# Performance work log

Hardware: AMD Instinct MI355X
Metric: run time of the kernel (lower is better)

## Reference

```python
import jax, jax.numpy as jnp
import numpy as np

NPOINT, RADIUS, NSAMPLE = 1024, 0.2, 32
BN_EPS = 1e-5


def _fps(xyz, npoint):
    """Farthest point sampling. xyz: [B,N,3] -> idx [B,npoint]. Deterministic seed (point 0)."""
    B, N, _ = xyz.shape
    init = (jnp.full((B, N), 1e10, xyz.dtype), jnp.zeros((B,), jnp.int32))

    def step(carry, _):
        distance, farthest = carry
        centroid = jnp.take_along_axis(xyz, farthest[:, None, None], axis=1)  # [B,1,3]
        dist = jnp.sum((xyz - centroid) ** 2, -1)                              # [B,N]
        distance = jnp.minimum(distance, dist)
        nxt = jnp.argmax(distance, axis=-1).astype(jnp.int32)
        return (distance, nxt), farthest

    _, cents = jax.lax.scan(step, init, None, length=npoint)  # [npoint,B]
    return cents.T  # [B,npoint]


def _gather(points, idx):
    """points [B,N,C], idx [B,...] -> [B,...,C] (batched fancy indexing)."""
    return jax.vmap(lambda p, i: p[i])(points, idx)


def _square_distance(src, dst):
    # [B,S,3] x [B,N,3] -> [B,S,N]
    d = -2.0 * jnp.einsum('bsc,bnc->bsn', src, dst)
    d += jnp.sum(src ** 2, -1)[:, :, None]
    d += jnp.sum(dst ** 2, -1)[:, None, :]
    return d


def _query_ball(radius, nsample, xyz, new_xyz):
    B, N, _ = xyz.shape
    sqr = _square_distance(new_xyz, xyz)                      # [B,S,N]
    base = jnp.arange(N, dtype=jnp.int32)[None, None, :]
    idx = jnp.where(sqr > radius ** 2, N, base)
    idx = jnp.sort(idx, axis=-1)[:, :, :nsample]              # [B,S,K]
    first = idx[:, :, 0:1]
    idx = jnp.where(idx == N, first, idx)
    return jnp.clip(idx, 0, N - 1)


def _mlp_bn_relu(h, w, b, g, be):
    # h: [B,S,K,Cin]; 1x1 conv == matmul; BN (training-mode batch stats) over (B,S,K).
    y = jnp.einsum('bskc,cd->bskd', h, w) + b
    mu = jnp.mean(y, axis=(0, 1, 2))
    var = jnp.var(y, axis=(0, 1, 2))
    y = (y - mu) * jax.lax.rsqrt(var + BN_EPS) * g + be
    return jax.nn.relu(y)


def setup_inputs():
    key = jax.random.key(0)
    ks = jax.random.split(key, 8)
    B, N, D = 16, 4096, 64
    xyz = jax.random.uniform(ks[0], (B, 3, N), jnp.float32)           # points in unit cube
    points = jax.random.normal(ks[1], (B, D, N), jnp.float32)
    c = [3 + D, 64, 64, 128]
    w0 = jax.random.normal(ks[2], (c[0], c[1]), jnp.float32) * 0.1
    w1 = jax.random.normal(ks[3], (c[1], c[2]), jnp.float32) * 0.1
    w2 = jax.random.normal(ks[4], (c[2], c[3]), jnp.float32) * 0.1
    b0 = jax.random.normal(ks[5], (c[1],), jnp.float32) * 0.05
    b1 = jax.random.normal(ks[6], (c[2],), jnp.float32) * 0.05
    b2 = jax.random.normal(ks[7], (c[3],), jnp.float32) * 0.05
    return dict(xyz=xyz, points=points,
                w0=w0, b0=b0, g0=jnp.ones(c[1]), be0=jnp.zeros(c[1]),
                w1=w1, b1=b1, g1=jnp.ones(c[2]), be1=jnp.zeros(c[2]),
                w2=w2, b2=b2, g2=jnp.ones(c[3]), be2=jnp.zeros(c[3]))


def reference(xyz, points, w0, b0, g0, be0, w1, b1, g1, be1, w2, b2, g2, be2):
    xyz_t = jnp.transpose(xyz, (0, 2, 1))       # [B,N,3]
    pts_t = jnp.transpose(points, (0, 2, 1))    # [B,N,D]
    B, N, _ = xyz_t.shape

    fps_idx = _fps(xyz_t, NPOINT)                               # [B,S]
    new_xyz = _gather(xyz_t, fps_idx)                           # [B,S,3]
    idx = _query_ball(RADIUS, NSAMPLE, xyz_t, new_xyz)          # [B,S,K]
    grouped_xyz = _gather(xyz_t, idx) - new_xyz[:, :, None, :]  # [B,S,K,3]
    grouped_pts = _gather(pts_t, idx)                           # [B,S,K,D]
    h = jnp.concatenate([grouped_xyz, grouped_pts], axis=-1)    # [B,S,K,3+D]

    h = _mlp_bn_relu(h, w0, b0, g0, be0)
    h = _mlp_bn_relu(h, w1, b1, g1, be1)
    h = _mlp_bn_relu(h, w2, b2, g2, be2)
    new_points = jnp.max(h, axis=2)                             # [B,S,Cout]

    return jnp.transpose(new_xyz, (0, 2, 1)), jnp.transpose(new_points, (0, 2, 1))
```

## Files before the change

### kernel.cpp

```cpp
#include <hip/hip_runtime.h>
#include <hip/hip_bf16.h>

typedef unsigned short u16;
typedef short short8 __attribute__((ext_vector_type(8)));
typedef float f32x4 __attribute__((ext_vector_type(4)));

#define NBLK_PASS 4096

#define WS_XYZT   0u
#define WS_PTSH   786432u
#define WS_PTSL   (WS_PTSH + 8388608u)
#define WS_NEWXYZ (WS_PTSL + 8388608u)
#define WS_BALL   (WS_NEWXYZ + 196608u)
#define WS_W0F    (WS_BALL + 2097152u)
#define WS_W1F    (WS_W0F + 24576u)
#define WS_W2F    (WS_W1F + 16384u)
#define WS_P0     (WS_W2F + 32768u)
#define WS_P1     (WS_P0 + 2097152u)
#define WS_P2     (WS_P1 + 2097152u)
#define WS_PR     (WS_P2 + 4194304u)
#define WS_AC0    (WS_PR + 65536u)
#define WS_AC1    (WS_AC0 + 1024u)
#define WS_AC2    (WS_AC1 + 1024u)

__device__ __forceinline__ void split2(float v, u16& h, u16& l) {
  __hip_bfloat16 bh = __float2bfloat16(v);
  float r = v - __bfloat162float(bh);
  __hip_bfloat16 bl = __float2bfloat16(r);
  h = *reinterpret_cast<u16*>(&bh);
  l = *reinterpret_cast<u16*>(&bl);
}

#define DPP_MAX64(CTRL) { \
  unsigned int lo_ = (unsigned int)k, hi_ = (unsigned int)(k >> 32); \
  unsigned int mlo_ = (unsigned int)__builtin_amdgcn_update_dpp(0, (int)lo_, CTRL, 0xF, 0xF, true); \
  unsigned int mhi_ = (unsigned int)__builtin_amdgcn_update_dpp(0, (int)hi_, CTRL, 0xF, 0xF, true); \
  unsigned long long m_ = ((unsigned long long)mhi_ << 32) | mlo_; \
  if (m_ > k) k = m_; }

__global__ __launch_bounds__(512) void front_k(
    const float* __restrict__ xyz, const float* __restrict__ pts,
    const float* __restrict__ w0, const float* __restrict__ w1, const float* __restrict__ w2,
    float* __restrict__ xyzT, u16* __restrict__ ptsH, u16* __restrict__ ptsL,
    float* __restrict__ newxyz, float* __restrict__ out0,
    u16* __restrict__ w0f, u16* __restrict__ w1f, u16* __restrict__ w2f)
{
  __shared__ __align__(16) char sm[53376];
  int bid = blockIdx.x, tid = threadIdx.x;

  if (bid < 16) {
    float* lx = (float*)sm; float* ly = lx + 4096; float* lz = ly + 4096;
    int* sIdx = (int*)(sm + 49152);
    unsigned long long* red = (unsigned long long*)(sm + 53248);
    int b = bid, lane = tid & 63, wid = tid >> 6;
    const float4* sx = (const float4*)(xyz + (size_t)(b*3 + 0)*4096);
    const float4* sy = (const float4*)(xyz + (size_t)(b*3 + 1)*4096);
    const float4* sz = (const float4*)(xyz + (size_t)(b*3 + 2)*4096);
    for (int i = tid; i < 1024; i += 512) {
      ((float4*)lx)[i] = sx[i]; ((float4*)ly)[i] = sy[i]; ((float4*)lz)[i] = sz[i];
    }
    __syncthreads();
    float px[8], py[8], pz[8], dist[8];
    #pragma unroll
    for (int i = 0; i < 8; ++i) {
      int p = tid + 512*i;
      px[i] = lx[p]; py[i] = ly[p]; pz[i] = lz[p]; dist[i] = 1e10f;
    }
    unsigned int lo0 = 4095u - (unsigned int)tid;
    int far = 0;
    for (int t = 0; t < 1024; ++t) {
      if (tid == 0) sIdx[t] = far;
      if (t == 1023) break;
      float cx = lx[far], cy = ly[far], cz = lz[far];
      float bestnd = -1.f; unsigned int bestlow = 0u;
      #pragma unroll
      for (int i = 0; i < 8; ++i) {
        float dx = __fsub_rn(px[i], cx);
        float dy = __fsub_rn(py[i], cy);
        float dz = __fsub_rn(pz[i], cz);
        float d = __fadd_rn(__fadd_rn(__fmul_rn(dx,dx), __fmul_rn(dy,dy)), __fmul_rn(dz,dz));
        float nd = fminf(dist[i], d);
        dist[i] = nd;
        if (nd > bestnd) { bestnd = nd; bestlow = lo0 - 512u*i; }
      }
      unsigned long long k = ((unsigned long long)__float_as_uint(bestnd) << 32) | bestlow;
      DPP_MAX64(0x111) DPP_MAX64(0x112) DPP_MAX64(0x114) DPP_MAX64(0x118)
      DPP_MAX64(0x142) DPP_MAX64(0x143)
      if (lane == 63) red[(t & 1)*8 + wid] = k;
      __syncthreads();
      const unsigned long long* rr = red + (t & 1)*8;
      unsigned long long m = rr[0];
      #pragma unroll
      for (int w = 1; w < 8; ++w) { unsigned long long o = rr[w]; if (o > m) m = o; }
      far = 4095 - (int)(unsigned int)(m & 0xffffffffull);
    }
    __syncthreads();
    for (int t = tid; t < 1024; t += 512) {
      int fi = sIdx[t];
      float x = lx[fi], y = ly[fi], z = lz[fi];
      size_t nb = ((size_t)b*1024 + t)*3;
      newxyz[nb + 0] = x; newxyz[nb + 1] = y; newxyz[nb + 2] = z;
      out0[(size_t)(b*3 + 0)*1024 + t] = x;
      out0[(size_t)(b*3 + 1)*1024 + t] = y;
      out0[(size_t)(b*3 + 2)*1024 + t] = z;
    }
  } else if (bid == 16) {
    for (int e = tid; e < 6144; e += 512) {
      int j = e & 7, l = (e >> 3) & 63, ct = (e >> 9) & 3, ks = e >> 11;
      int kk = ks*32 + (l >> 4)*8 + j, col = ct*16 + (l & 15);
      float v = 0.f;
      if (kk < 67) { int orow = (kk < 64) ? (kk + 3) : (kk - 64); v = w0[orow*64 + col]; }
      u16 h, lo; split2(v, h, lo);
      w0f[e] = h; w0f[6144 + e] = lo;
    }
    for (int e = tid; e < 4096; e += 512) {
      int j = e & 7, l = (e >> 3) & 63, ct = (e >> 9) & 3, ks = e >> 11;
      int kk = ks*32 + (l >> 4)*8 + j, col = ct*16 + (l & 15);
      u16 h, lo; split2(w1[kk*64 + col], h, lo);
      w1f[e] = h; w1f[4096 + e] = lo;
    }
    for (int e = tid; e < 8192; e += 512) {
      int j = e & 7, l = (e >> 3) & 63, ct = (e >> 9) & 3, ks = (e >> 11) & 1, cg = e >> 12;
      int kk = ks*32 + (l >> 4)*8 + j, col = cg*64 + ct*16 + (l & 15);
      u16 h, lo; split2(w2[kk*128 + col], h, lo);
      w2f[e] = h; w2f[8192 + e] = lo;
    }
  } else if (bid < 145) {
    int i = (bid - 17)*512 + tid;
    int b = i >> 12, n = i & 4095;
    float x = xyz[(b*3 + 0)*4096 + n];
    float y = xyz[(b*3 + 1)*4096 + n];
    float z = xyz[(b*3 + 2)*4096 + n];
    xyzT[(size_t)i*3 + 0] = x; xyzT[(size_t)i*3 + 1] = y; xyzT[(size_t)i*3 + 2] = z;
  } else {
    int bx = bid - 145;
    u16* th = (u16*)sm;
    u16* tl = th + 64*68;
    int b = bx >> 6, nt = bx & 63;
    int j = tid & 63, dq = tid >> 6;
    #pragma unroll
    for (int db = 0; db < 8; ++db) {
      int d = db*8 + dq;
      float v = pts[((size_t)(b*64 + d))*4096 + nt*64 + j];
      u16 h, lo; split2(v, h, lo);
      th[j*68 + d] = h; tl[j*68 + d] = lo;
    }
    __syncthreads();
    int row = tid >> 3, q = tid & 7;
    size_t o = ((size_t)(b*4096 + nt*64 + row))*64 + q*8;
    const u16* sh = th + row*68 + q*8;
    const u16* sl = tl + row*68 + q*8;
    uint2 h0 = *(const uint2*)(sh), h1 = *(const uint2*)(sh + 4);
    uint2 l0 = *(const uint2*)(sl), l1 = *(const uint2*)(sl + 4);
    *(uint2*)(ptsH + o) = h0; *(uint2*)(ptsH + o + 4) = h1;
    *(uint2*)(ptsL + o) = l0; *(uint2*)(ptsL + o + 4) = l1;
  }
}

__global__ __launch_bounds__(256) void ball_k(const float* __restrict__ xyz,
                                              const float* __restrict__ newxyz,
                                              int* __restrict__ ballidx) {
  __shared__ __align__(16) float lx[4096], ly[4096], lz[4096], ldn[4096];
  int b = blockIdx.x >> 5, tid = threadIdx.x, lane = tid & 63, wid = tid >> 6;
  const float4* sx = (const float4*)(xyz + (size_t)(b*3 + 0)*4096);
  const float4* sy = (const float4*)(xyz + (size_t)(b*3 + 1)*4096);
  const float4* sz = (const float4*)(xyz + (size_t)(b*3 + 2)*4096);
  for (int i = tid; i < 1024; i += 256) {
    ((float4*)lx)[i] = sx[i]; ((float4*)ly)[i] = sy[i]; ((float4*)lz)[i] = sz[i];
  }
  __syncthreads();
  for (int i = tid; i < 4096; i += 256) {
    float x = lx[i], y = ly[i], z = lz[i];
    ldn[i] = __fadd_rn(__fadd_rn(__fmul_rn(x,x), __fmul_rn(y,y)), __fmul_rn(z,z));
  }
  __syncthreads();
  int s0 = (blockIdx.x & 31)*32 + wid*8;
  for (int ci = 0; ci < 8; ++ci) {
    int s = s0 + ci;
    const float* cp = newxyz + ((size_t)b*1024 + s)*3;
    float cx = cp[0], cy = cp[1], cz = cp[2];
    float sn = __fadd_rn(__fadd_rn(__fmul_rn(cx,cx), __fmul_rn(cy,cy)), __fmul_rn(cz,cz));
    int* orow = ballidx + (((size_t)b << 10) + s)*32;
    int cnt = 0, first = -1;
    for (int ch = 0; ch < 64; ++ch) {
      int p = ch*64 + lane;
      float x = lx[p], y = ly[p], z = lz[p];
      float dot = __fmaf_rn(cz, z, __fmaf_rn(cy, y, __fmul_rn(cx, x)));
      float sqr = __fadd_rn(__fadd_rn(__fmul_rn(-2.0f, dot), sn), ldn[p]);
      bool in = !(sqr > 0.04f);
      unsigned long long mask = __ballot(in);
      if (first < 0 && mask) first = ch*64 + (__ffsll((long long)mask) - 1);
      int rank = cnt + __popcll(mask & ((1ull << lane) - 1ull));
      if (in && rank < 32) orow[rank] = p;
      cnt += __popcll(mask);
      if (cnt >= 32) break;
    }
    if (cnt < 32) {
      int fv = (first < 0) ? 4095 : first;
      if (lane >= cnt && lane < 32) orow[lane] = fv;
    }
  }
}

#define LOFF 6144

__device__ __forceinline__ void stats_fin(float* sSt, float* __restrict__ partial,
                                          int C, int tid, int bid) {
  __syncthreads();
  for (int c = tid; c < C; c += 256) {
    float s = sSt[c*2] + sSt[(128 + c)*2] + sSt[(256 + c)*2] + sSt[(384 + c)*2];
    float q = sSt[c*2 + 1] + sSt[(128 + c)*2 + 1] + sSt[(256 + c)*2 + 1] + sSt[(384 + c)*2 + 1];
    partial[(size_t)bid*2*C + c] = s;
    partial[(size_t)bid*2*C + C + c] = q;
  }
}

template<int DEPTH>
__global__ __launch_bounds__(256, 2) void pass_k(
    const int* __restrict__ ballidx,
    const u16* __restrict__ ptsH, const u16* __restrict__ ptsL,
    const float* __restrict__ xyzT, const float* __restrict__ newxyz,
    const u16* __restrict__ w0f, const u16* __restrict__ w1f, const u16* __restrict__ w2f,
    const float* __restrict__ b0, const float* __restrict__ b1, const float* __restrict__ b2,
    const float* __restrict__ ac0, const float* __restrict__ ac1, const float* __restrict__ ac2,
    float* __restrict__ partial, float* __restrict__ outPts)
{
  __shared__ __align__(16) u16 sAh[128*104];
  __shared__ __align__(16) u16 sAl[128*104];
  __shared__ __align__(16) u16 sW[12288];
  int tid = threadIdx.x, lane = tid & 63, wid = tid >> 6;
  int lrow = lane & 15, lkg = lane >> 4;
  int r0 = wid*32;

  {
    int r = tid >> 1, half = tid & 1;
    int R = blockIdx.x*128 + r;
    int b = R >> 15, s = (R & 32767) >> 5;
    int n = ballidx[R];
    size_t o = ((((size_t)b << 12) + n) << 6) + half*32;
    const uint4* srcH = (const uint4*)(ptsH + o);
    const uint4* srcL = (const uint4*)(ptsL + o);
    uint4* dH = (uint4*)(&sAh[r*104 + half*32]);
    uint4* dL = (uint4*)(&sAl[r*104 + half*32]);
    #pragma unroll
    for (int i = 0; i < 4; ++i) { dH[i] = srcH[i]; dL[i] = srcL[i]; }
    if (half) {
      uint4 zz; zz.x = zz.y = zz.z = zz.w = 0u;
      uint4* zH = (uint4*)(&sAh[r*104 + 64]);
      uint4* zL = (uint4*)(&sAl[r*104 + 64]);
      #pragma unroll
      for (int i = 0; i < 4; ++i) { zH[i] = zz; zL[i] = zz; }
      const float* xp = xyzT + (((size_t)b << 12) + n)*3;
      const float* cp = newxyz + (((size_t)b << 10) + s)*3;
      #pragma unroll
      for (int d = 0; d < 3; ++d) {
        u16 h, l; split2(__fsub_rn(xp[d], cp[d]), h, l);
        sAh[r*104 + 64 + d] = h; sAl[r*104 + 64 + d] = l;
      }
    }
  }
  for (int i = tid; i < 768; i += 256) {
    ((uint4*)sW)[i] = ((const uint4*)w0f)[i];
    *(uint4*)(sW + LOFF + i*8) = ((const uint4*)(w0f + 6144))[i];
  }
  __syncthreads();

  f32x4 zv = {0.f, 0.f, 0.f, 0.f};

  f32x4 acc[2][4];
  #pragma unroll
  for (int rt = 0; rt < 2; ++rt)
    #pragma unroll
    for (int ct = 0; ct < 4; ++ct) acc[rt][ct] = zv;
  #pragma unroll
  for (int ks = 0; ks < 3; ++ks) {
    short8 ah[2], al[2];
    #pragma unroll
    for (int rt = 0; rt < 2; ++rt) {
      int ro = (r0 + rt*16 + lrow)*104 + ks*32 + lkg*8;
      ah[rt] = *(const short8*)&sAh[ro];
      al[rt] = *(const short8*)&sAl[ro];
    }
    #pragma unroll
    for (int ct = 0; ct < 4; ++ct) {
      short8 wh = *(const short8*)&sW[((ks*4 + ct)*64 + lane)*8];
      short8 wl = *(const short8*)&sW[LOFF + ((ks*4 + ct)*64 + lane)*8];
      #pragma unroll
      for (int rt = 0; rt < 2; ++rt) {
        acc[rt][ct] = __builtin_amdgcn_mfma_f32_16x16x32_bf16(ah[rt], wh, acc[rt][ct], 0, 0, 0);
        acc[rt][ct] = __builtin_amdgcn_mfma_f32_16x16x32_bf16(al[rt], wh, acc[rt][ct], 0, 0, 0);
        acc[rt][ct] = __builtin_amdgcn_mfma_f32_16x16x32_bf16(ah[rt], wl, acc[rt][ct], 0, 0, 0);
      }
    }
  }

  if constexpr (DEPTH == 1) {
    __syncthreads();
    float* sSt = (float*)sW;
    #pragma unroll
    for (int ct = 0; ct < 4; ++ct) {
      int col = ct*16 + lrow;
      float bv = b0[col], s = 0.f, q = 0.f;
      #pragma unroll
      for (int rt = 0; rt < 2; ++rt)
        #pragma unroll
        for (int r = 0; r < 4; ++r) { float v = acc[rt][ct][r] + bv; s += v; q += v*v; }
      s += __shfl_xor(s, 16, 64); q += __shfl_xor(q, 16, 64);
      s += __shfl_xor(s, 32, 64); q += __shfl_xor(q, 32, 64);
      if (lane < 16) { sSt[(wid*128 + col)*2] = s; sSt[(wid*128 + col)*2 + 1] = q; }
    }
    stats_fin(sSt, partial, 64, tid, blockIdx.x);
    return;
  } else {
    __syncthreads();
    #pragma unroll
    for (int ct = 0; ct < 4; ++ct) {
      int col = ct*16 + lrow;
      float a = ac0[col], cc = fmaf(a, b0[col], ac0[64 + col]);
      #pragma unroll
      for (int rt = 0; rt < 2; ++rt)
        #pragma unroll
        for (int r = 0; r < 4; ++r) {
          float v = fmaxf(fmaf(a, acc[rt][ct][r], cc), 0.f);
          int row = r0 + rt*16 + lkg*4 + r;
          u16 h, l; split2(v, h, l);
          sAh[row*72 + col] = h; sAl[row*72 + col] = l;
        }
    }
    for (int i = tid; i < 512; i += 256) {
      ((uint4*)sW)[i] = ((const uint4*)w1f)[i];
      *(uint4*)(sW + LOFF + i*8) = ((const uint4*)(w1f + 4096))[i];
    }
    __syncthreads();

    #pragma unroll
    for (int rt = 0; rt < 2; ++rt)
      #pragma unroll
      for (int ct = 0; ct < 4; ++ct) acc[rt][ct] = zv;
    #pragma unroll
    for (int ks = 0; ks < 2; ++ks) {
      short8 ah[2], al[2];
      #pragma unroll
      for (int rt = 0; rt < 2; ++rt) {
        int ro = (r0 + rt*16 + lrow)*72 + ks*32 + lkg*8;
        ah[rt] = *(const short8*)&sAh[ro];
        al[rt] = *(const short8*)&sAl[ro];
      }
      #pragma unroll
      for (int ct = 0; ct < 4; ++ct) {
        short8 wh = *(const short8*)&sW[((ks*4 + ct)*64 + lane)*8];
        short8 wl = *(const short8*)&sW[LOFF + ((ks*4 + ct)*64 + lane)*8];
        #pragma unroll
        for (int rt = 0; rt < 2; ++rt) {
          acc[rt][ct] = __builtin_amdgcn_mfma_f32_16x16x32_bf16(ah[rt], wh, acc[rt][ct], 0, 0, 0);
          acc[rt][ct] = __builtin_amdgcn_mfma_f32_16x16x32_bf16(al[rt], wh, acc[rt][ct], 0, 0, 0);
          acc[rt][ct] = __builtin_amdgcn_mfma_f32_16x16x32_bf16(ah[rt], wl, acc[rt][ct], 0, 0, 0);
        }
      }
    }

    if constexpr (DEPTH == 2) {
      __syncthreads();
      float* sSt = (float*)sW;
      #pragma unroll
      for (int ct = 0; ct < 4; ++ct) {
        int col = ct*16 + lrow;
        float bv = b1[col], s = 0.f, q = 0.f;
        #pragma unroll
        for (int rt = 0; rt < 2; ++rt)
          #pragma unroll
          for (int r = 0; r < 4; ++r) { float v = acc[rt][ct][r] + bv; s += v; q += v*v; }
        s += __shfl_xor(s, 16, 64); q += __shfl_xor(q, 16, 64);
        s += __shfl_xor(s, 32, 64); q += __shfl_xor(q, 32, 64);
        if (lane < 16) { sSt[(wid*128 + col)*2] = s; sSt[(wid*128 + col)*2 + 1] = q; }
      }
      stats_fin(sSt, partial, 64, tid, blockIdx.x);
      return;
    } else {
      __syncthreads();
      #pragma unroll
      for (int ct = 0; ct < 4; ++ct) {
        int col = ct*16 + lrow;
        float a = ac1[col], cc = fmaf(a, b1[col], ac1[64 + col]);
        #pragma unroll
        for (int rt = 0; rt < 2; ++rt)
          #pragma unroll
          for (int r = 0; r < 4; ++r) {
            float v = fmaxf(fmaf(a, acc[rt][ct][r], cc), 0.f);
            int row = r0 + rt*16 + lkg*4 + r;
            u16 h, l; split2(v, h, l);
            sAh[row*72 + col] = h; sAl[row*72 + col] = l;
          }
      }
      for (int i = tid; i < 512; i += 256) {
        ((uint4*)sW)[i] = ((const uint4*)w2f)[i];
        *(uint4*)(sW + LOFF + i*8) = ((const uint4*)(w2f + 8192))[i];
      }
      __syncthreads();

      float sc[2][4], sq[2][4];
      #pragma unroll
      for (int cg = 0; cg < 2; ++cg) {
        if (cg) {
          __syncthreads();
          for (int i = tid; i < 512; i += 256) {
            ((uint4*)sW)[i] = ((const uint4*)(w2f + 4096))[i];
            *(uint4*)(sW + LOFF + i*8) = ((const uint4*)(w2f + 12288))[i];
          }
          __syncthreads();
        }
        f32x4 acc2[2][4];
        #pragma unroll
        for (int rt = 0; rt < 2; ++rt)
          #pragma unroll
          for (int ct = 0; ct < 4; ++ct) acc2[rt][ct] = zv;
        #pragma unroll
        for (int ks = 0; ks < 2; ++ks) {
          short8 ah[2], al[2];
          #pragma unroll
          for (int rt = 0; rt < 2; ++rt) {
            int ro = (r0 + rt*16 + lrow)*72 + ks*32 + lkg*8;
            ah[rt] = *(const short8*)&sAh[ro];
            al[rt] = *(const short8*)&sAl[ro];
          }
          #pragma unroll
          for (int ct = 0; ct < 4; ++ct) {
            short8 wh = *(const short8*)&sW[((ks*4 + ct)*64 + lane)*8];
            short8 wl = *(const short8*)&sW[LOFF + ((ks*4 + ct)*64 + lane)*8];
            #pragma unroll
            for (int rt = 0; rt < 2; ++rt) {
              acc2[rt][ct] = __builtin_amdgcn_mfma_f32_16x16x32_bf16(ah[rt], wh, acc2[rt][ct], 0, 0, 0);
              acc2[rt][ct] = __builtin_amdgcn_mfma_f32_16x16x32_bf16(al[rt], wh, acc2[rt][ct], 0, 0, 0);
              acc2[rt][ct] = __builtin_amdgcn_mfma_f32_16x16x32_bf16(ah[rt], wl, acc2[rt][ct], 0, 0, 0);
            }
          }
        }
        if constexpr (DEPTH == 3) {
          #pragma unroll
          for (int ct = 0; ct < 4; ++ct) {
            int col = cg*64 + ct*16 + lrow;
            float bv = b2[col], s = 0.f, q = 0.f;
            #pragma unroll
            for (int rt = 0; rt < 2; ++rt)
              #pragma unroll
              for (int r = 0; r < 4; ++r) { float v = acc2[rt][ct][r] + bv; s += v; q += v*v; }
            s += __shfl_xor(s, 16, 64); q += __shfl_xor(q, 16, 64);
            s += __shfl_xor(s, 32, 64); q += __shfl_xor(q, 32, 64);
            sc[cg][ct] = s; sq[cg][ct] = q;
          }
        } else {
          int G = blockIdx.x*4 + wid;
          int bb = G >> 10, ss = G & 1023;
          #pragma unroll
          for (int ct = 0; ct < 4; ++ct) {
            int col = cg*64 + ct*16 + lrow;
            float a = ac2[col], cc = fmaf(a, b2[col], ac2[128 + col]);
            float m = 0.f;
            #pragma unroll
            for (int rt = 0; rt < 2; ++rt)
              #pragma unroll
              for (int r = 0; r < 4; ++r)
                m = fmaxf(m, fmaxf(fmaf(a, acc2[rt][ct][r], cc), 0.f));
            m = fmaxf(m, __shfl_xor(m, 16, 64));
            m = fmaxf(m, __shfl_xor(m, 32, 64));
            if (lane < 16) outPts[((size_t)bb*128 + col)*1024 + ss] = m;
          }
        }
      }
      if constexpr (DEPTH == 3) {
        __syncthreads();
        float* sSt = (float*)sW;
        if (lane < 16) {
          #pragma unroll
          for (int cg = 0; cg < 2; ++cg)
            #pragma unroll
            for (int ct = 0; ct < 4; ++ct) {
              int col = cg*64 + ct*16 + lrow;
              sSt[(wid*128 + col)*2] = sc[cg][ct];
              sSt[(wid*128 + col)*2 + 1] = sq[cg][ct];
            }
        }
        stats_fin(sSt, partial, 128, tid, blockIdx.x);
      }
    }
  }
}

__global__ void r1_k(const float* __restrict__ partial, int C, float* __restrict__ pr) {
  int j = blockIdx.x, c = threadIdx.x;
  if (c < 2*C) {
    float s = 0.f;
    for (int i = 0; i < 64; ++i) s += partial[((size_t)(j*64 + i))*2*C + c];
    pr[j*2*C + c] = s;
  }
}
__global__ void r2_k(const float* __restrict__ pr, int C,
                     const float* __restrict__ g, const float* __restrict__ be,
                     float* __restrict__ ac) {
  int c = threadIdx.x;
  if (c < C) {
    float s = 0.f, q = 0.f;
    for (int j = 0; j < 64; ++j) { s += pr[j*2*C + c]; q += pr[j*2*C + C + c]; }
    const float inv = 1.0f / 524288.0f;
    float mu = s*inv, var = q*inv - mu*mu;
    float a = g[c] / sqrtf(var + 1e-5f);
    ac[c] = a; ac[C + c] = be[c] - mu*a;
  }
}

extern "C" void kernel_launch(void* const* d_in, const int* in_sizes, int n_in,
                              void* d_out, int out_size, void* d_ws, size_t ws_size,
                              hipStream_t stream) {
  const float* xyz = (const float*)d_in[0];
  const float* pts = (const float*)d_in[1];
  const float* w0  = (const float*)d_in[2];
  const float* b0  = (const float*)d_in[3];
  const float* g0  = (const float*)d_in[4];
  const float* be0 = (const float*)d_in[5];
  const float* w1  = (const float*)d_in[6];
  const float* b1  = (const float*)d_in[7];
  const float* g1  = (const float*)d_in[8];
  const float* be1 = (const float*)d_in[9];
  const float* w2  = (const float*)d_in[10];
  const float* b2  = (const float*)d_in[11];
  const float* g2  = (const float*)d_in[12];
  const float* be2 = (const float*)d_in[13];
  float* out = (float*)d_out;
  char* ws = (char*)d_ws;

  float* xyzT   = (float*)(ws + WS_XYZT);
  u16*   ptsH   = (u16*)(ws + WS_PTSH);
  u16*   ptsL   = (u16*)(ws + WS_PTSL);
  float* newxyz = (float*)(ws + WS_NEWXYZ);
  int*   ballix = (int*)(ws + WS_BALL);
  u16*   w0f    = (u16*)(ws + WS_W0F);
  u16*   w1f    = (u16*)(ws + WS_W1F);
  u16*   w2f    = (u16*)(ws + WS_W2F);
  float* p0     = (float*)(ws + WS_P0);
  float* p1     = (float*)(ws + WS_P1);
  float* p2     = (float*)(ws + WS_P2);
  float* pr     = (float*)(ws + WS_PR);
  float* ac0    = (float*)(ws + WS_AC0);
  float* ac1    = (float*)(ws + WS_AC1);
  float* ac2    = (float*)(ws + WS_AC2);
  float* outPts = out + 49152;

  front_k<<<1169, 512, 0, stream>>>(xyz, pts, w0, w1, w2, xyzT, ptsH, ptsL,
                                    newxyz, out, w0f, w1f, w2f);
  ball_k<<<512, 256, 0, stream>>>(xyz, newxyz, ballix);

  pass_k<1><<<NBLK_PASS, 256, 0, stream>>>(ballix, ptsH, ptsL, xyzT, newxyz,
      w0f, w1f, w2f, b0, b1, b2, ac0, ac1, ac2, p0, outPts);
  r1_k<<<64, 256, 0, stream>>>(p0, 64, pr);
  r2_k<<<1, 256, 0, stream>>>(pr, 64, g0, be0, ac0);

  pass_k<2><<<NBLK_PASS, 256, 0, stream>>>(ballix, ptsH, ptsL, xyzT, newxyz,
      w0f, w1f, w2f, b0, b1, b2, ac0, ac1, ac2, p1, outPts);
  r1_k<<<64, 256, 0, stream>>>(p1, 64, pr);
  r2_k<<<1, 256, 0, stream>>>(pr, 64, g1, be1, ac1);

  pass_k<3><<<NBLK_PASS, 256, 0, stream>>>(ballix, ptsH, ptsL, xyzT, newxyz,
      w0f, w1f, w2f, b0, b1, b2, ac0, ac1, ac2, p2, outPts);
  r1_k<<<64, 256, 0, stream>>>(p2, 128, pr);
  r2_k<<<1, 256, 0, stream>>>(pr, 128, g2, be2, ac2);

  pass_k<4><<<NBLK_PASS, 256, 0, stream>>>(ballix, ptsH, ptsL, xyzT, newxyz,
      w0f, w1f, w2f, b0, b1, b2, ac0, ac1, ac2, p2, outPts);
}
```

Before: 1.128 ms.

## Pack two FPS batches per block with per-group shared-memory barriers

The farthest-point-sampling stage now runs two batches per 512-thread block, 256 threads each holding 16 points, instead of one batch per block. It replaces the block-wide __syncthreads with a custom per-group barrier built on a shared atomic counter and a generation flag, so each half-block syncs only its own 4 waves. The aim is to cut the cost of the 1023 serial reduction barriers and halve the number of FPS blocks. In exchange it adds spin-wait traffic, doubles shared memory per block, and does twice the per-thread work per iteration.

Result: slower. 1.310 ms (+16.2%).

```diff
diff --git a/kernel.cpp b/kernel.cpp
--- a/kernel.cpp
+++ b/kernel.cpp
@@ -31,80 +31,106 @@
   l = *reinterpret_cast<u16*>(&bl);
 }
 
-#define DPP_MAX64(CTRL) { \
-  unsigned int lo_ = (unsigned int)k, hi_ = (unsigned int)(k >> 32); \
+#define DPP_MAX64(K, CTRL) { \
+  unsigned int lo_ = (unsigned int)(K), hi_ = (unsigned int)((K) >> 32); \
   unsigned int mlo_ = (unsigned int)__builtin_amdgcn_update_dpp(0, (int)lo_, CTRL, 0xF, 0xF, true); \
   unsigned int mhi_ = (unsigned int)__builtin_amdgcn_update_dpp(0, (int)hi_, CTRL, 0xF, 0xF, true); \
   unsigned long long m_ = ((unsigned long long)mhi_ << 32) | mlo_; \
-  if (m_ > k) k = m_; }
-
-__global__ __launch_bounds__(512) void front_k(
+  if (m_ > (K)) (K) = m_; }
+
+#define DPP_CHAIN(K) \
+  DPP_MAX64(K, 0x111) DPP_MAX64(K, 0x112) DPP_MAX64(K, 0x114) DPP_MAX64(K, 0x118) \
+  DPP_MAX64(K, 0x142) DPP_MAX64(K, 0x143)
+
+__global__ __launch_bounds__(512, 1) void front_k(
     const float* __restrict__ xyz, const float* __restrict__ pts,
     const float* __restrict__ w0, const float* __restrict__ w1, const float* __restrict__ w2,
     float* __restrict__ xyzT, u16* __restrict__ ptsH, u16* __restrict__ ptsL,
     float* __restrict__ newxyz, float* __restrict__ out0,
     u16* __restrict__ w0f, u16* __restrict__ w1f, u16* __restrict__ w2f)
 {
-  __shared__ __align__(16) char sm[53376];
+  __shared__ __align__(16) char sm[106656];
   int bid = blockIdx.x, tid = threadIdx.x;
 
-  if (bid < 16) {
-    float* lx = (float*)sm; float* ly = lx + 4096; float* lz = ly + 4096;
-    int* sIdx = (int*)(sm + 49152);
-    unsigned long long* red = (unsigned long long*)(sm + 53248);
-    int b = bid, lane = tid & 63, wid = tid >> 6;
-    const float4* sx = (const float4*)(xyz + (size_t)(b*3 + 0)*4096);
-    const float4* sy = (const float4*)(xyz + (size_t)(b*3 + 1)*4096);
-    const float4* sz = (const float4*)(xyz + (size_t)(b*3 + 2)*4096);
-    for (int i = tid; i < 1024; i += 512) {
+  if (bid < 8) {
+    int g = tid >> 8, gtid = tid & 255;
+    int lane = tid & 63, wid4 = (tid >> 6) & 3;
+    int batch = bid*2 + g;
+    float* lx = (float*)sm + (size_t)g*12288;
+    float* ly = lx + 4096;
+    float* lz = ly + 4096;
+    int* sIdx = (int*)(sm + 98304) + g*1024;
+    unsigned long long* red = (unsigned long long*)(sm + 106496) + g*8;
+    unsigned* sctr = (unsigned*)(sm + 106624);
+    unsigned* sgen = sctr + 2;
+
+    if (tid < 2) { sctr[tid] = 0u; sgen[tid] = 0u; }
+
+    const float4* sx = (const float4*)(xyz + (size_t)(batch*3 + 0)*4096);
+    const float4* sy = (const float4*)(xyz + (size_t)(batch*3 + 1)*4096);
+    const float4* sz = (const float4*)(xyz + (size_t)(batch*3 + 2)*4096);
+    for (int i = gtid; i < 1024; i += 256) {
       ((float4*)lx)[i] = sx[i]; ((float4*)ly)[i] = sy[i]; ((float4*)lz)[i] = sz[i];
     }
     __syncthreads();
-    float px[8], py[8], pz[8], dist[8];
-    #pragma unroll
-    for (int i = 0; i < 8; ++i) {
-      int p = tid + 512*i;
+
+    float px[16], py[16], pz[16], dist[16];
+    #pragma unroll
+    for (int i = 0; i < 16; ++i) {
+      int p = gtid + 256*i;
       px[i] = lx[p]; py[i] = ly[p]; pz[i] = lz[p]; dist[i] = 1e10f;
     }
-    unsigned int lo0 = 4095u - (unsigned int)tid;
+    unsigned int lo0 = 4095u - (unsigned int)gtid;
     int far = 0;
     for (int t = 0; t < 1024; ++t) {
-      if (tid == 0) sIdx[t] = far;
+      if (gtid == 0) sIdx[t] = far;
       if (t == 1023) break;
       float cx = lx[far], cy = ly[far], cz = lz[far];
       float bestnd = -1.f; unsigned int bestlow = 0u;
       #pragma unroll
-      for (int i = 0; i < 8; ++i) {
+      for (int i = 0; i < 16; ++i) {
         float dx = __fsub_rn(px[i], cx);
         float dy = __fsub_rn(py[i], cy);
         float dz = __fsub_rn(pz[i], cz);
         float d = __fadd_rn(__fadd_rn(__fmul_rn(dx,dx), __fmul_rn(dy,dy)), __fmul_rn(dz,dz));
         float nd = fminf(dist[i], d);
         dist[i] = nd;
-        if (nd > bestnd) { bestnd = nd; bestlow = lo0 - 512u*i; }
+        if (nd > bestnd) { bestnd = nd; bestlow = lo0 - 256u*i; }
       }
       unsigned long long k = ((unsigned long long)__float_as_uint(bestnd) << 32) | bestlow;
-      DPP_MAX64(0x111) DPP_MAX64(0x112) DPP_MAX64(0x114) DPP_MAX64(0x118)
-      DPP_MAX64(0x142) DPP_MAX64(0x143)
-      if (lane == 63) red[(t & 1)*8 + wid] = k;
-      __syncthreads();
-      const unsigned long long* rr = red + (t & 1)*8;
+      DPP_CHAIN(k)
+      if (lane == 63) red[(t & 1)*4 + wid4] = k;
+      {
+        __threadfence_block();
+        unsigned gen = ((volatile unsigned*)sgen)[g];
+        asm volatile("" ::: "memory");
+        if (lane == 0) {
+          unsigned old = atomicAdd(&sctr[g], 1u);
+          if (old == 3u) {
+            sctr[g] = 0u;
+            __threadfence_block();
+            ((volatile unsigned*)sgen)[g] = gen + 1u;
+          }
+        }
+        while (((volatile unsigned*)sgen)[g] == gen) __builtin_amdgcn_s_sleep(1);
+      }
+      const unsigned long long* rr = red + (t & 1)*4;
       unsigned long long m = rr[0];
       #pragma unroll
-      for (int w = 1; w < 8; ++w) { unsigned long long o = rr[w]; if (o > m) m = o; }
+      for (int w = 1; w < 4; ++w) { unsigned long long o = rr[w]; if (o > m) m = o; }
       far = 4095 - (int)(unsigned int)(m & 0xffffffffull);
     }
     __syncthreads();
-    for (int t = tid; t < 1024; t += 512) {
+    for (int t = gtid; t < 1024; t += 256) {
       int fi = sIdx[t];
       float x = lx[fi], y = ly[fi], z = lz[fi];
-      size_t nb = ((size_t)b*1024 + t)*3;
+      size_t nb = ((size_t)batch*1024 + t)*3;
       newxyz[nb + 0] = x; newxyz[nb + 1] = y; newxyz[nb + 2] = z;
-      out0[(size_t)(b*3 + 0)*1024 + t] = x;
-      out0[(size_t)(b*3 + 1)*1024 + t] = y;
-      out0[(size_t)(b*3 + 2)*1024 + t] = z;
-    }
-  } else if (bid == 16) {
+      out0[(size_t)(batch*3 + 0)*1024 + t] = x;
+      out0[(size_t)(batch*3 + 1)*1024 + t] = y;
+      out0[(size_t)(batch*3 + 2)*1024 + t] = z;
+    }
+  } else if (bid == 8) {
     for (int e = tid; e < 6144; e += 512) {
       int j = e & 7, l = (e >> 3) & 63, ct = (e >> 9) & 3, ks = e >> 11;
       int kk = ks*32 + (l >> 4)*8 + j, col = ct*16 + (l & 15);
@@ -125,15 +151,15 @@
       u16 h, lo; split2(w2[kk*128 + col], h, lo);
       w2f[e] = h; w2f[8192 + e] = lo;
     }
-  } else if (bid < 145) {
-    int i = (bid - 17)*512 + tid;
+  } else if (bid < 137) {
+    int i = (bid - 9)*512 + tid;
     int b = i >> 12, n = i & 4095;
     float x = xyz[(b*3 + 0)*4096 + n];
     float y = xyz[(b*3 + 1)*4096 + n];
     float z = xyz[(b*3 + 2)*4096 + n];
     xyzT[(size_t)i*3 + 0] = x; xyzT[(size_t)i*3 + 1] = y; xyzT[(size_t)i*3 + 2] = z;
   } else {
-    int bx = bid - 145;
+    int bx = bid - 137;
     u16* th = (u16*)sm;
     u16* tl = th + 64*68;
     int b = bx >> 6, nt = bx & 63;
@@ -545,7 +571,7 @@
   float* ac2    = (float*)(ws + WS_AC2);
   float* outPts = out + 49152;
 
-  front_k<<<1169, 512, 0, stream>>>(xyz, pts, w0, w1, w2, xyzT, ptsH, ptsL,
+  front_k<<<1161, 512, 0, stream>>>(xyz, pts, w0, w1, w2, xyzT, ptsH, ptsL,
                                     newxyz, out, w0f, w1f, w2f);
   ball_k<<<512, 256, 0, stream>>>(xyz, newxyz, ballix);
 
```
